# Performance work log

Measured on AMD Instinct MI355X. Metric: run time of the kernel, lower is better.

## Reference

```python
import jax, jax.numpy as jnp
import numpy as np

EPS = 1e-5
C = 1.0
SQRT_C = 1.0
MAX_NORM = 0.95


def _log0(y):
    # log map at origin: atanh(sqrt(c)||y||) * y / (sqrt(c)||y||)
    norm = jnp.clip(jnp.linalg.norm(y, axis=-1, keepdims=True), EPS)
    arg = jnp.clip(SQRT_C * norm, None, 1.0 - EPS)
    return jnp.arctanh(arg) * y / (SQRT_C * norm)


def _exp0(v):
    # exp map at origin: tanh(sqrt(c)||v||) * v / (sqrt(c)||v||)
    norm = jnp.clip(jnp.linalg.norm(v, axis=-1, keepdims=True), EPS)
    return jnp.tanh(SQRT_C * norm) * v / (SQRT_C * norm)


def _proj(x):
    # project onto Poincare ball of radius MAX_NORM/sqrt(c)
    max_r = MAX_NORM / SQRT_C
    norm = jnp.linalg.norm(x, axis=-1, keepdims=True)
    return jnp.where(norm > max_r, x * max_r / jnp.clip(norm, EPS), x)


def _hyp_linear(x, W, b):
    # log -> euclidean linear -> exp -> project
    v = _log0(x)
    v = v @ W.T + b
    return _proj(_exp0(v))


def _hyp_graph_conv(x, src, dst, n_nodes, Wm, bm, Wu, bu):
    # 1. hyperbolic linear message transform
    h = _hyp_linear(x, Wm, bm)
    # 2. tangent-space (hyperbolic) mean aggregation over incoming edges
    t = _log0(h[src])                                   # [E, D]
    summed = jax.ops.segment_sum(t, dst, num_segments=n_nodes)
    cnt = jax.ops.segment_sum(jnp.ones((src.shape[0], 1), t.dtype), dst,
                              num_segments=n_nodes)
    agg = _proj(_exp0(summed / jnp.clip(cnt, 1.0)))
    # 3. hyperbolic linear update
    return _hyp_linear(agg, Wu, bu)


def setup_inputs() -> dict:
    key = jax.random.key(0)
    k1, k2, k3, k4 = jax.random.split(key, 4)
    N, E, D, L = 50000, 800000, 128, 2
    x = jax.random.normal(k1, (N, D), dtype=jnp.float32) * 0.01
    edge_index = jax.random.randint(k2, (2, E), 0, N, dtype=jnp.int32)
    msg_W = jax.random.normal(k3, (L, D, D), dtype=jnp.float32) * 0.05
    msg_b = jnp.zeros((L, D), dtype=jnp.float32)
    upd_W = jax.random.normal(k4, (L, D, D), dtype=jnp.float32) * 0.05
    upd_b = jnp.zeros((L, D), dtype=jnp.float32)
    return {"x": x, "edge_index": edge_index, "msg_W": msg_W, "msg_b": msg_b,
            "upd_W": upd_W, "upd_b": upd_b}


def reference(x, edge_index, msg_W, msg_b, upd_W, upd_b):
    src, dst = edge_index[0], edge_index[1]
    n_nodes = x.shape[0]
    h = x
    for l in range(msg_W.shape[0]):  # small fixed layer count
        h = _hyp_graph_conv(h, src, dst, n_nodes,
                            msg_W[l], msg_b[l], upd_W[l], upd_b[l])
    return h
```

## Files before the change

kernel.cpp:

```cpp
#include <hip/hip_runtime.h>
#include <math.h>

#define EPSF 1e-5f
#define MAXN 0.95f
#define DD 128

typedef unsigned short u16;
typedef __attribute__((ext_vector_type(8))) __bf16 bf16x8;
typedef __attribute__((ext_vector_type(4))) float f32x4;
typedef __attribute__((ext_vector_type(8))) unsigned short u16x8;
typedef __attribute__((ext_vector_type(4))) unsigned u32x4;

#define MFMA16 __builtin_amdgcn_mfma_f32_16x16x32_bf16

__device__ __forceinline__ u16 f2bf(float f) {
    unsigned u = __float_as_uint(f);
    return (u16)((u + 0x7FFFu + ((u >> 16) & 1u)) >> 16);
}
__device__ __forceinline__ float bf2f(u16 b) {
    return __uint_as_float(((unsigned)b) << 16);
}

__device__ __forceinline__ float chain_scale(float nrm, bool log_out) {
    float nc  = fmaxf(nrm, EPSF);
    float f   = tanhf(nc) / nc;
    float wn  = f * nrm;
    float p   = (wn > MAXN) ? (MAXN / fmaxf(wn, EPSF)) : 1.f;
    float s   = f * p;
    if (log_out) {
        float n2  = wn * p;
        float n2c = fmaxf(n2, EPSF);
        float arg = fminf(n2c, 1.f - EPSF);
        s *= atanhf(arg) / n2c;
    }
    return s;
}

__device__ __forceinline__ float agg_scale(const float* __restrict__ ssum,
                                           const int* __restrict__ rowptr,
                                           int rg) {
    int cnt = max(rowptr[rg + 1] - rowptr[rg], 1);
    float inv = 1.f / (float)cnt;
    return chain_scale(sqrtf(ssum[rg]) * inv, true) * inv;
}

__global__ __launch_bounds__(256)
void zero_int4(int4* __restrict__ p, int n4)
{
    int i = blockIdx.x * 256 + threadIdx.x;
    if (i < n4) p[i] = make_int4(0, 0, 0, 0);
}

__global__ __launch_bounds__(256)
void split_w(const float* __restrict__ msgW, const float* __restrict__ updW,
             u16* __restrict__ whi, u16* __restrict__ wlo, int L)
{
    int gid = blockIdx.x * 256 + threadIdx.x;
    int total = L * 2 * DD * DD;
    if (gid >= total) return;
    int mat = gid >> 14;
    int elem = gid & (DD * DD - 1);
    int l = mat >> 1, tpe = mat & 1;
    float f = (tpe ? updW : msgW)[(size_t)l * DD * DD + elem];
    u16 hb = f2bf(f);
    whi[gid] = hb;
    wlo[gid] = f2bf(f - bf2f(hb));
}

template<int LOG_OUT, int FP32_OUT, int F32_IN, int SCALE_IN>
__global__ __launch_bounds__(256)
void mfma_linear(const u16* __restrict__ vhi, const float* __restrict__ xin,
                 const float* __restrict__ ssum, const int* __restrict__ rowptr,
                 const u16* __restrict__ whi, const u16* __restrict__ wlo,
                 const float* __restrict__ bias,
                 u16* __restrict__ ohi, float* __restrict__ ofp, int N)
{
    __shared__ float sred[4][64];
    __shared__ float sScale[64];
    __shared__ float sSin[SCALE_IN ? 64 : 1];
    __shared__ u16 sHi[FP32_OUT ? 1 : 64][136];

    const int tid  = threadIdx.x;
    const int w    = tid >> 6;
    const int lane = tid & 63;
    const int l15  = lane & 15, lk = lane >> 4;
    const int base = blockIdx.x * 64;

    if (SCALE_IN) {
        if (tid < 64) {
            int rg = base + tid;
            sSin[tid] = agg_scale(ssum, rowptr, rg < N ? rg : (N - 1));
        }
        __syncthreads();
    }

    bf16x8 wh[2][4], wl[2][4];
    #pragma unroll
    for (int nt = 0; nt < 2; ++nt) {
        const int j = w * 32 + nt * 16 + l15;
        #pragma unroll
        for (int kt = 0; kt < 4; ++kt) {
            const int off = j * DD + kt * 32 + lk * 8;
            wh[nt][kt] = *(const bf16x8*)(whi + off);
            wl[nt][kt] = *(const bf16x8*)(wlo + off);
        }
    }
    const float bv0 = bias[w * 32 + l15];
    const float bv1 = bias[w * 32 + 16 + l15];

    f32x4 acc[4][2];
    #pragma unroll
    for (int mt = 0; mt < 4; ++mt)
        #pragma unroll
        for (int nt = 0; nt < 2; ++nt)
            acc[mt][nt] = (f32x4){0.f, 0.f, 0.f, 0.f};

    #pragma unroll
    for (int mt = 0; mt < 4; ++mt) {
        int row = base + mt * 16 + l15;
        row = (row < N) ? row : (N - 1);
        bf16x8 ah[4];
        if (F32_IN) {
            const float* xr = xin + (size_t)row * DD + lk * 8;
            float fv[32];
            float ss = 0.f;
            #pragma unroll
            for (int kt = 0; kt < 4; ++kt) {
                float4 a = *(const float4*)(xr + kt * 32);
                float4 b = *(const float4*)(xr + kt * 32 + 4);
                fv[kt*8+0]=a.x; fv[kt*8+1]=a.y; fv[kt*8+2]=a.z; fv[kt*8+3]=a.w;
                fv[kt*8+4]=b.x; fv[kt*8+5]=b.y; fv[kt*8+6]=b.z; fv[kt*8+7]=b.w;
            }
            #pragma unroll
            for (int q = 0; q < 32; ++q) ss += fv[q] * fv[q];
            ss += __shfl_xor(ss, 16);
            ss += __shfl_xor(ss, 32);
            float nc = fmaxf(sqrtf(ss), EPSF);
            float sc = atanhf(fminf(nc, 1.f - EPSF)) / nc;
            #pragma unroll
            for (int kt = 0; kt < 4; ++kt) {
                u16x8 uh;
                #pragma unroll
                for (int q = 0; q < 8; ++q)
                    uh[q] = f2bf(fv[kt*8+q] * sc);
                ah[kt] = *reinterpret_cast<bf16x8*>(&uh);
            }
        } else {
            const size_t ro = (size_t)row * DD + lk * 8;
            #pragma unroll
            for (int kt = 0; kt < 4; ++kt)
                ah[kt] = *(const bf16x8*)(vhi + ro + kt * 32);
        }
        #pragma unroll
        for (int kt = 0; kt < 4; ++kt) {
            #pragma unroll
            for (int nt = 0; nt < 2; ++nt) {
                acc[mt][nt] = MFMA16(ah[kt], wh[nt][kt], acc[mt][nt], 0, 0, 0);
                acc[mt][nt] = MFMA16(ah[kt], wl[nt][kt], acc[mt][nt], 0, 0, 0);
            }
        }
    }

    #pragma unroll
    for (int mt = 0; mt < 4; ++mt) {
        #pragma unroll
        for (int r = 0; r < 4; ++r) {
            const float sv = SCALE_IN ? sSin[mt*16 + lk*4 + r] : 1.f;
            float y0 = acc[mt][0][r] * sv + bv0;
            float y1 = acc[mt][1][r] * sv + bv1;
            float part = y0 * y0 + y1 * y1;
            part += __shfl_xor(part, 1);
            part += __shfl_xor(part, 2);
            part += __shfl_xor(part, 4);
            part += __shfl_xor(part, 8);
            if (l15 == 0) sred[w][mt*16 + lk*4 + r] = part;
        }
    }
    __syncthreads();
    if (tid < 64) {
        float ss = sred[0][tid] + sred[1][tid] + sred[2][tid] + sred[3][tid];
        sScale[tid] = chain_scale(sqrtf(ss), LOG_OUT != 0);
    }
    __syncthreads();

    #pragma unroll
    for (int mt = 0; mt < 4; ++mt) {
        #pragma unroll
        for (int r = 0; r < 4; ++r) {
            const int rloc = mt*16 + lk*4 + r;
            const float s = sScale[rloc];
            const float sv = SCALE_IN ? sSin[rloc] : 1.f;
            #pragma unroll
            for (int nt = 0; nt < 2; ++nt) {
                float z = (acc[mt][nt][r] * sv + (nt ? bv1 : bv0)) * s;
                const int col = w*32 + nt*16 + l15;
                if (FP32_OUT) {
                    const int rg = base + rloc;
                    if (rg < N) ofp[(size_t)rg * DD + col] = z;
                } else {
                    sHi[rloc][col] = f2bf(z);
                }
            }
        }
    }
    if (!FP32_OUT) {
        __syncthreads();
        const int row = tid >> 2, qc = (tid & 3) * 32;
        const int rg = base + row;
        if (rg < N) {
            #pragma unroll
            for (int i = 0; i < 4; ++i)
                *(u16x8*)(ohi + (size_t)rg * DD + qc + i*8) =
                    *(const u16x8*)(&sHi[row][qc + i*8]);
        }
    }
}

__global__ __launch_bounds__(256)
void mfma_linear_fused(const u16* __restrict__ vhi,
                       const float* __restrict__ ssum, const int* __restrict__ rowptr,
                       const u16* __restrict__ wuh, const u16* __restrict__ wul,
                       const float* __restrict__ bu,
                       const u16* __restrict__ wmh, const u16* __restrict__ wml,
                       const float* __restrict__ bm,
                       u16* __restrict__ ohi, int N)
{
    __shared__ float sred[4][64];
    __shared__ float sScale[64];
    __shared__ float sSin[64];
    __shared__ u16 sHi[64][136];

    const int tid  = threadIdx.x;
    const int w    = tid >> 6;
    const int lane = tid & 63;
    const int l15  = lane & 15, lk = lane >> 4;
    const int base = blockIdx.x * 64;

    if (tid < 64) {
        int rg = base + tid;
        sSin[tid] = agg_scale(ssum, rowptr, rg < N ? rg : (N - 1));
    }
    __syncthreads();

    f32x4 acc[4][2];

    {
        bf16x8 wh[2][4], wl[2][4];
        #pragma unroll
        for (int nt = 0; nt < 2; ++nt) {
            const int j = w * 32 + nt * 16 + l15;
            #pragma unroll
            for (int kt = 0; kt < 4; ++kt) {
                const int off = j * DD + kt * 32 + lk * 8;
                wh[nt][kt] = *(const bf16x8*)(wuh + off);
                wl[nt][kt] = *(const bf16x8*)(wul + off);
            }
        }
        const float bv0 = bu[w * 32 + l15];
        const float bv1 = bu[w * 32 + 16 + l15];

        #pragma unroll
        for (int mt = 0; mt < 4; ++mt)
            #pragma unroll
            for (int nt = 0; nt < 2; ++nt)
                acc[mt][nt] = (f32x4){0.f, 0.f, 0.f, 0.f};

        #pragma unroll
        for (int mt = 0; mt < 4; ++mt) {
            int row = base + mt * 16 + l15;
            row = (row < N) ? row : (N - 1);
            const size_t ro = (size_t)row * DD + lk * 8;
            bf16x8 ah[4];
            #pragma unroll
            for (int kt = 0; kt < 4; ++kt)
                ah[kt] = *(const bf16x8*)(vhi + ro + kt * 32);
            #pragma unroll
            for (int kt = 0; kt < 4; ++kt) {
                #pragma unroll
                for (int nt = 0; nt < 2; ++nt) {
                    acc[mt][nt] = MFMA16(ah[kt], wh[nt][kt], acc[mt][nt], 0, 0, 0);
                    acc[mt][nt] = MFMA16(ah[kt], wl[nt][kt], acc[mt][nt], 0, 0, 0);
                }
            }
        }

        #pragma unroll
        for (int mt = 0; mt < 4; ++mt) {
            #pragma unroll
            for (int r = 0; r < 4; ++r) {
                const float sv = sSin[mt*16 + lk*4 + r];
                float y0 = acc[mt][0][r] * sv + bv0;
                float y1 = acc[mt][1][r] * sv + bv1;
                float part = y0 * y0 + y1 * y1;
                part += __shfl_xor(part, 1);
                part += __shfl_xor(part, 2);
                part += __shfl_xor(part, 4);
                part += __shfl_xor(part, 8);
                if (l15 == 0) sred[w][mt*16 + lk*4 + r] = part;
            }
        }
        __syncthreads();
        if (tid < 64) {
            float ss = sred[0][tid] + sred[1][tid] + sred[2][tid] + sred[3][tid];
            sScale[tid] = chain_scale(sqrtf(ss), true);
        }
        __syncthreads();
        #pragma unroll
        for (int mt = 0; mt < 4; ++mt) {
            #pragma unroll
            for (int r = 0; r < 4; ++r) {
                const int rloc = mt*16 + lk*4 + r;
                const float s = sScale[rloc];
                const float sv = sSin[rloc];
                #pragma unroll
                for (int nt = 0; nt < 2; ++nt) {
                    float z = (acc[mt][nt][r] * sv + (nt ? bv1 : bv0)) * s;
                    sHi[rloc][w*32 + nt*16 + l15] = f2bf(z);
                }
            }
        }
    }
    __syncthreads();

    {
        bf16x8 wh[2][4], wl[2][4];
        #pragma unroll
        for (int nt = 0; nt < 2; ++nt) {
            const int j = w * 32 + nt * 16 + l15;
            #pragma unroll
            for (int kt = 0; kt < 4; ++kt) {
                const int off = j * DD + kt * 32 + lk * 8;
                wh[nt][kt] = *(const bf16x8*)(wmh + off);
                wl[nt][kt] = *(const bf16x8*)(wml + off);
            }
        }
        const float bv0 = bm[w * 32 + l15];
        const float bv1 = bm[w * 32 + 16 + l15];

        #pragma unroll
        for (int mt = 0; mt < 4; ++mt)
            #pragma unroll
            for (int nt = 0; nt < 2; ++nt)
                acc[mt][nt] = (f32x4){0.f, 0.f, 0.f, 0.f};

        #pragma unroll
        for (int mt = 0; mt < 4; ++mt) {
            const int r16 = mt * 16 + l15;
            bf16x8 ah[4];
            #pragma unroll
            for (int kt = 0; kt < 4; ++kt)
                ah[kt] = *(const bf16x8*)(&sHi[r16][kt * 32 + lk * 8]);
            #pragma unroll
            for (int kt = 0; kt < 4; ++kt) {
                #pragma unroll
                for (int nt = 0; nt < 2; ++nt) {
                    acc[mt][nt] = MFMA16(ah[kt], wh[nt][kt], acc[mt][nt], 0, 0, 0);
                    acc[mt][nt] = MFMA16(ah[kt], wl[nt][kt], acc[mt][nt], 0, 0, 0);
                }
            }
        }

        #pragma unroll
        for (int mt = 0; mt < 4; ++mt) {
            #pragma unroll
            for (int r = 0; r < 4; ++r) {
                float y0 = acc[mt][0][r] + bv0;
                float y1 = acc[mt][1][r] + bv1;
                float part = y0 * y0 + y1 * y1;
                part += __shfl_xor(part, 1);
                part += __shfl_xor(part, 2);
                part += __shfl_xor(part, 4);
                part += __shfl_xor(part, 8);
                if (l15 == 0) sred[w][mt*16 + lk*4 + r] = part;
            }
        }
        __syncthreads();
        if (tid < 64) {
            float ss = sred[0][tid] + sred[1][tid] + sred[2][tid] + sred[3][tid];
            sScale[tid] = chain_scale(sqrtf(ss), true);
        }
        __syncthreads();
        #pragma unroll
        for (int mt = 0; mt < 4; ++mt) {
            #pragma unroll
            for (int r = 0; r < 4; ++r) {
                const int rloc = mt*16 + lk*4 + r;
                const float s = sScale[rloc];
                #pragma unroll
                for (int nt = 0; nt < 2; ++nt) {
                    float z = (acc[mt][nt][r] + (nt ? bv1 : bv0)) * s;
                    sHi[rloc][w*32 + nt*16 + l15] = f2bf(z);
                }
            }
        }
        __syncthreads();
        const int row = tid >> 2, qc = (tid & 3) * 32;
        const int rg = base + row;
        if (rg < N) {
            #pragma unroll
            for (int i = 0; i < 4; ++i)
                *(u16x8*)(ohi + (size_t)rg * DD + qc + i*8) =
                    *(const u16x8*)(&sHi[row][qc + i*8]);
        }
    }
}

__global__ __launch_bounds__(256)
void degree_rank(const int* __restrict__ dst, int* __restrict__ deg,
                 int* __restrict__ rank, int E)
{
    int e4 = (blockIdx.x * 256 + threadIdx.x) * 4;
    if (e4 + 3 < E) {
        int4 d = *(const int4*)(dst + e4);
        int4 r;
        r.x = atomicAdd(&deg[d.x], 1);
        r.y = atomicAdd(&deg[d.y], 1);
        r.z = atomicAdd(&deg[d.z], 1);
        r.w = atomicAdd(&deg[d.w], 1);
        *(int4*)(rank + e4) = r;
    } else {
        for (int e = e4; e < E; ++e) rank[e] = atomicAdd(&deg[dst[e]], 1);
    }
}

__global__ __launch_bounds__(1024)
void scan_rowptr(const int* __restrict__ deg, int* __restrict__ rowptr, int N)
{
    __shared__ int wsum[16];
    const int t = threadIdx.x, wv = t >> 6, ln = t & 63;
    int carry = 0;
    const int nch = (N + 4095) / 4096;
    for (int c = 0; c < nch; ++c) {
        const int i = c * 4096 + t * 4;
        int4 d = *(const int4*)(deg + i);
        int e1 = d.x, e2 = e1 + d.y, e3 = e2 + d.z, tot = e3 + d.w;
        int sc = tot;
        #pragma unroll
        for (int off = 1; off < 64; off <<= 1) {
            int u = __shfl_up(sc, off);
            if (ln >= off) sc += u;
        }
        if (ln == 63) wsum[wv] = sc;
        __syncthreads();
        if (wv == 0 && ln < 16) {
            int s2 = wsum[ln];
            #pragma unroll
            for (int off = 1; off < 16; off <<= 1) {
                int u = __shfl_up(s2, off);
                if (ln >= off) s2 += u;
            }
            wsum[ln] = s2;
        }
        __syncthreads();
        const int off0 = carry + ((wv > 0) ? wsum[wv - 1] : 0) + (sc - tot);
        if (i + 3 < N) {
            *(int4*)(rowptr + i) = make_int4(off0, off0 + e1, off0 + e2, off0 + e3);
        } else {
            if (i     < N) rowptr[i]     = off0;
            if (i + 1 < N) rowptr[i + 1] = off0 + e1;
            if (i + 2 < N) rowptr[i + 2] = off0 + e2;
        }
        carry += wsum[15];
        __syncthreads();
    }
    if (t == 0) rowptr[N] = carry;
}

__global__ __launch_bounds__(256)
void fill_csr(const int* __restrict__ src, const int* __restrict__ dst,
              const int* __restrict__ rowptr, const int* __restrict__ rank,
              int* __restrict__ csr, int E)
{
    int e4 = (blockIdx.x * 256 + threadIdx.x) * 4;
    if (e4 + 3 < E) {
        int4 d = *(const int4*)(dst + e4);
        int4 r = *(const int4*)(rank + e4);
        int4 s = *(const int4*)(src + e4);
        csr[rowptr[d.x] + r.x] = s.x;
        csr[rowptr[d.y] + r.y] = s.y;
        csr[rowptr[d.z] + r.z] = s.z;
        csr[rowptr[d.w] + r.w] = s.w;
    } else {
        for (int e = e4; e < E; ++e) csr[rowptr[dst[e]] + rank[e]] = src[e];
    }
}

__global__ __launch_bounds__(256)
void csr_gather_sum(const u16* __restrict__ ghi, const int* __restrict__ rowptr,
                    const int* __restrict__ csr, u16* __restrict__ ohi,
                    float* __restrict__ ssum, int N)
{
    int node = blockIdx.x * 4 + (threadIdx.x >> 6);
    if (node >= N) return;
    const int lane = threadIdx.x & 63;
    const int eg = lane >> 4, l15 = lane & 15;
    const int beg = rowptr[node], end = rowptr[node + 1];

    float acc[8] = {0.f,0.f,0.f,0.f,0.f,0.f,0.f,0.f};
    for (int b = beg; b < end; b += 64) {
        const int cnt = min(end - b, 64);
        const int myidx = (lane < cnt) ? csr[b + lane] : 0;
        u32x4 vc;
        {
            const bool act = eg < cnt;
            const int s = __shfl(myidx, act ? eg : 0);
            if (act) vc = *(const u32x4*)(ghi + (size_t)s * DD + l15 * 8);
        }
        for (int j = 0; j < cnt; j += 4) {
            const int en = j + 4 + eg;
            const bool actn = en < cnt;
            const int sn = __shfl(myidx, actn ? en : 0);
            u32x4 vn;
            if (actn) vn = *(const u32x4*)(ghi + (size_t)sn * DD + l15 * 8);
            if (j + eg < cnt) {
                #pragma unroll
                for (int p = 0; p < 4; ++p) {
                    acc[2*p+0] += __uint_as_float(vc[p] << 16);
                    acc[2*p+1] += __uint_as_float(vc[p] & 0xffff0000u);
                }
            }
            vc = vn;
        }
    }
    #pragma unroll
    for (int q = 0; q < 8; ++q) {
        acc[q] += __shfl_xor(acc[q], 16);
        acc[q] += __shfl_xor(acc[q], 32);
    }
    float ss = 0.f;
    #pragma unroll
    for (int q = 0; q < 8; ++q) ss += acc[q] * acc[q];
    ss += __shfl_xor(ss, 1); ss += __shfl_xor(ss, 2);
    ss += __shfl_xor(ss, 4); ss += __shfl_xor(ss, 8);
    if (eg == 0) {
        u32x4 hw;
        #pragma unroll
        for (int p = 0; p < 4; ++p) {
            u16 h0 = f2bf(acc[2*p+0]), h1 = f2bf(acc[2*p+1]);
            hw[p] = (unsigned)h0 | ((unsigned)h1 << 16);
        }
        *(u32x4*)(ohi + (size_t)node * DD + l15 * 8) = hw;
        if (l15 == 0) ssum[node] = ss;
    }
}

extern "C" void kernel_launch(void* const* d_in, const int* in_sizes, int n_in,
                              void* d_out, int out_size, void* d_ws, size_t ws_size,
                              hipStream_t stream)
{
    const float* x     = (const float*)d_in[0];
    const int*   ei    = (const int*)d_in[1];
    const float* msg_W = (const float*)d_in[2];
    const float* msg_b = (const float*)d_in[3];
    const float* upd_W = (const float*)d_in[4];
    const float* upd_b = (const float*)d_in[5];

    const int N = in_sizes[0] / DD;
    const int E = in_sizes[1] / 2;
    const int L = in_sizes[2] / (DD * DD);

    const int* src = ei;
    const int* dst = ei + E;

    u16* Ahi  = (u16*)d_ws;
    u16* WhiA = Ahi + (size_t)N * DD;
    u16* WloA = WhiA + (size_t)2 * L * DD * DD;
    int* deg  = (int*)(WloA + (size_t)2 * L * DD * DD);
    const int degCap = ((N + 4095) / 4096) * 4096;
    int* rowptr = deg + degCap;
    int* csr    = rowptr + (N + 1);
    float* ssum = (float*)(csr + E);

    u16* Bhi  = (u16*)d_out;
    int* rank = (int*)(Bhi + (size_t)N * DD);

    const int nodeBlocks  = (N + 63) / 64;
    const int aggBlocks   = (N + 3) / 4;
    const int edge4Blocks = ((E + 3) / 4 + 255) / 256;

    zero_int4<<<(degCap / 4 + 255) / 256, 256, 0, stream>>>((int4*)deg, degCap / 4);
    degree_rank<<<edge4Blocks, 256, 0, stream>>>(dst, deg, rank, E);
    scan_rowptr<<<1, 1024, 0, stream>>>(deg, rowptr, N);
    fill_csr<<<edge4Blocks, 256, 0, stream>>>(src, dst, rowptr, rank, csr, E);
    split_w<<<(2 * L * DD * DD + 255) / 256, 256, 0, stream>>>(
        msg_W, upd_W, WhiA, WloA, L);

    mfma_linear<1, 0, 1, 0><<<nodeBlocks, 256, 0, stream>>>(
        nullptr, x, nullptr, nullptr,
        WhiA, WloA, msg_b, Bhi, nullptr, N);

    for (int l = 0; l < L; ++l) {
        const u16* wuh = WhiA + (size_t)(l * 2 + 1) * DD * DD;
        const u16* wul = WloA + (size_t)(l * 2 + 1) * DD * DD;

        csr_gather_sum<<<aggBlocks, 256, 0, stream>>>(
            Bhi, rowptr, csr, Ahi, ssum, N);

        if (l < L - 1) {
            const u16* wmh = WhiA + (size_t)((l + 1) * 2 + 0) * DD * DD;
            const u16* wml = WloA + (size_t)((l + 1) * 2 + 0) * DD * DD;
            mfma_linear_fused<<<nodeBlocks, 256, 0, stream>>>(
                Ahi, ssum, rowptr,
                wuh, wul, upd_b + (size_t)l * DD,
                wmh, wml, msg_b + (size_t)(l + 1) * DD,
                Bhi, N);
        } else {
            mfma_linear<0, 1, 0, 1><<<nodeBlocks, 256, 0, stream>>>(
                Ahi, nullptr, ssum, rowptr,
                wuh, wul, upd_b + (size_t)l * DD,
                nullptr, (float*)d_out, N);
        }
    }
}
```

Baseline: 237.5 us.

## Build CSR with 16-bit packed edges and per-block shared-memory histograms

When N fits in 16 bits, edge indices are first packed to u16. Degree counting and CSR fill then run in 64 blocks, and each block scans all edges but owns one contiguous node range. Counts go through shared-memory atomics instead of global atomics, and no per-edge rank array is written. Each block rereads the full packed edge list, so total reads rise about 64-fold, and only 64 blocks are used. Fill order within a row becomes nondeterministic.

```diff
diff --git a/kernel.cpp b/kernel.cpp
--- a/kernel.cpp
+++ b/kernel.cpp
@@ -4,6 +4,7 @@
 #define EPSF 1e-5f
 #define MAXN 0.95f
 #define DD 128
+#define HBLK 64
 
 typedef unsigned short u16;
 typedef __attribute__((ext_vector_type(8))) __bf16 bf16x8;
@@ -405,6 +406,89 @@
     }
 }
 
+__global__ __launch_bounds__(512)
+void pack_u16(const int* __restrict__ ei, u16* __restrict__ s16,
+              u16* __restrict__ d16, int E)
+{
+    int e4 = (blockIdx.x * 512 + threadIdx.x) * 4;
+    if (e4 + 3 < E) {
+        int4 s = *(const int4*)(ei + e4);
+        int4 d = *(const int4*)(ei + E + e4);
+        ushort4 sp; sp.x = (u16)s.x; sp.y = (u16)s.y; sp.z = (u16)s.z; sp.w = (u16)s.w;
+        ushort4 dp; dp.x = (u16)d.x; dp.y = (u16)d.y; dp.z = (u16)d.z; dp.w = (u16)d.w;
+        *(ushort4*)(s16 + e4) = sp;
+        *(ushort4*)(d16 + e4) = dp;
+    } else {
+        for (int e = e4; e < E; ++e) {
+            s16[e] = (u16)ei[e];
+            d16[e] = (u16)ei[E + e];
+        }
+    }
+}
+
+__global__ __launch_bounds__(512)
+void deg_hist(const u16* __restrict__ d16, int* __restrict__ deg, int E, int N)
+{
+    __shared__ int hist[1032];
+    const int R  = (N + HBLK - 1) / HBLK;
+    const int lo = blockIdx.x * R;
+    const int hi = min(lo + R, N);
+    for (int j = threadIdx.x; j < R; j += 512) hist[j] = 0;
+    __syncthreads();
+    const int E8 = E >> 3;
+    for (int i = threadIdx.x; i < E8; i += 512) {
+        u16x8 v = *(const u16x8*)(d16 + i * 8);
+        #pragma unroll
+        for (int q = 0; q < 8; ++q) {
+            int d = v[q];
+            if (d >= lo && d < hi) atomicAdd(&hist[d - lo], 1);
+        }
+    }
+    for (int e = E8 * 8 + threadIdx.x; e < E; e += 512) {
+        int d = d16[e];
+        if (d >= lo && d < hi) atomicAdd(&hist[d - lo], 1);
+    }
+    __syncthreads();
+    for (int j = threadIdx.x; j < hi - lo; j += 512) deg[lo + j] = hist[j];
+}
+
+__global__ __launch_bounds__(512)
+void fill_hist(const u16* __restrict__ d16, const u16* __restrict__ s16,
+               const int* __restrict__ rowptr, int* __restrict__ csr,
+               int E, int N)
+{
+    __shared__ int rp[1032];
+    __shared__ int cnt[1032];
+    const int R  = (N + HBLK - 1) / HBLK;
+    const int lo = blockIdx.x * R;
+    const int hi = min(lo + R, N);
+    for (int j = threadIdx.x; j < hi - lo; j += 512) {
+        rp[j]  = rowptr[lo + j];
+        cnt[j] = 0;
+    }
+    __syncthreads();
+    const int E8 = E >> 3;
+    for (int i = threadIdx.x; i < E8; i += 512) {
+        u16x8 d = *(const u16x8*)(d16 + i * 8);
+        u16x8 s = *(const u16x8*)(s16 + i * 8);
+        #pragma unroll
+        for (int q = 0; q < 8; ++q) {
+            int dd = d[q];
+            if (dd >= lo && dd < hi) {
+                int pos = rp[dd - lo] + atomicAdd(&cnt[dd - lo], 1);
+                csr[pos] = (int)s[q];
+            }
+        }
+    }
+    for (int e = E8 * 8 + threadIdx.x; e < E; e += 512) {
+        int dd = d16[e];
+        if (dd >= lo && dd < hi) {
+            int pos = rp[dd - lo] + atomicAdd(&cnt[dd - lo], 1);
+            csr[pos] = (int)s16[e];
+        }
+    }
+}
+
 __global__ __launch_bounds__(256)
 void degree_rank(const int* __restrict__ dst, int* __restrict__ deg,
                  int* __restrict__ rank, int E)
@@ -423,49 +507,6 @@
     }
 }
 
-__global__ __launch_bounds__(1024)
-void scan_rowptr(const int* __restrict__ deg, int* __restrict__ rowptr, int N)
-{
-    __shared__ int wsum[16];
-    const int t = threadIdx.x, wv = t >> 6, ln = t & 63;
-    int carry = 0;
-    const int nch = (N + 4095) / 4096;
-    for (int c = 0; c < nch; ++c) {
-        const int i = c * 4096 + t * 4;
-        int4 d = *(const int4*)(deg + i);
-        int e1 = d.x, e2 = e1 + d.y, e3 = e2 + d.z, tot = e3 + d.w;
-        int sc = tot;
-        #pragma unroll
-        for (int off = 1; off < 64; off <<= 1) {
-            int u = __shfl_up(sc, off);
-            if (ln >= off) sc += u;
-        }
-        if (ln == 63) wsum[wv] = sc;
-        __syncthreads();
-        if (wv == 0 && ln < 16) {
-            int s2 = wsum[ln];
-            #pragma unroll
-            for (int off = 1; off < 16; off <<= 1) {
-                int u = __shfl_up(s2, off);
-                if (ln >= off) s2 += u;
-            }
-            wsum[ln] = s2;
-        }
-        __syncthreads();
-        const int off0 = carry + ((wv > 0) ? wsum[wv - 1] : 0) + (sc - tot);
-        if (i + 3 < N) {
-            *(int4*)(rowptr + i) = make_int4(off0, off0 + e1, off0 + e2, off0 + e3);
-        } else {
-            if (i     < N) rowptr[i]     = off0;
-            if (i + 1 < N) rowptr[i + 1] = off0 + e1;
-            if (i + 2 < N) rowptr[i + 2] = off0 + e2;
-        }
-        carry += wsum[15];
-        __syncthreads();
-    }
-    if (t == 0) rowptr[N] = carry;
-}
-
 __global__ __launch_bounds__(256)
 void fill_csr(const int* __restrict__ src, const int* __restrict__ dst,
               const int* __restrict__ rowptr, const int* __restrict__ rank,
@@ -483,6 +524,49 @@
     } else {
         for (int e = e4; e < E; ++e) csr[rowptr[dst[e]] + rank[e]] = src[e];
     }
+}
+
+__global__ __launch_bounds__(1024)
+void scan_rowptr(const int* __restrict__ deg, int* __restrict__ rowptr, int N)
+{
+    __shared__ int wsum[16];
+    const int t = threadIdx.x, wv = t >> 6, ln = t & 63;
+    int carry = 0;
+    const int nch = (N + 4095) / 4096;
+    for (int c = 0; c < nch; ++c) {
+        const int i = c * 4096 + t * 4;
+        int4 d = *(const int4*)(deg + i);
+        int e1 = d.x, e2 = e1 + d.y, e3 = e2 + d.z, tot = e3 + d.w;
+        int sc = tot;
+        #pragma unroll
+        for (int off = 1; off < 64; off <<= 1) {
+            int u = __shfl_up(sc, off);
+            if (ln >= off) sc += u;
+        }
+        if (ln == 63) wsum[wv] = sc;
+        __syncthreads();
+        if (wv == 0 && ln < 16) {
+            int s2 = wsum[ln];
+            #pragma unroll
+            for (int off = 1; off < 16; off <<= 1) {
+                int u = __shfl_up(s2, off);
+                if (ln >= off) s2 += u;
+            }
+            wsum[ln] = s2;
+        }
+        __syncthreads();
+        const int off0 = carry + ((wv > 0) ? wsum[wv - 1] : 0) + (sc - tot);
+        if (i + 3 < N) {
+            *(int4*)(rowptr + i) = make_int4(off0, off0 + e1, off0 + e2, off0 + e3);
+        } else {
+            if (i     < N) rowptr[i]     = off0;
+            if (i + 1 < N) rowptr[i + 1] = off0 + e1;
+            if (i + 2 < N) rowptr[i + 2] = off0 + e2;
+        }
+        carry += wsum[15];
+        __syncthreads();
+    }
+    if (t == 0) rowptr[N] = carry;
 }
 
 __global__ __launch_bounds__(256)
@@ -570,6 +654,8 @@
     int* rowptr = deg + degCap;
     int* csr    = rowptr + (N + 1);
     float* ssum = (float*)(csr + E);
+    u16* d16    = (u16*)(ssum + N);
+    u16* s16    = d16 + E;
 
     u16* Bhi  = (u16*)d_out;
     int* rank = (int*)(Bhi + (size_t)N * DD);
@@ -577,11 +663,22 @@
     const int nodeBlocks  = (N + 63) / 64;
     const int aggBlocks   = (N + 3) / 4;
     const int edge4Blocks = ((E + 3) / 4 + 255) / 256;
-
-    zero_int4<<<(degCap / 4 + 255) / 256, 256, 0, stream>>>((int4*)deg, degCap / 4);
-    degree_rank<<<edge4Blocks, 256, 0, stream>>>(dst, deg, rank, E);
-    scan_rowptr<<<1, 1024, 0, stream>>>(deg, rowptr, N);
-    fill_csr<<<edge4Blocks, 256, 0, stream>>>(src, dst, rowptr, rank, csr, E);
+    const bool u16ok = (N <= 65535) && ((N + HBLK - 1) / HBLK <= 1032);
+
+    if (u16ok) {
+        const int padStart4 = (N & ~3) / 4;
+        zero_int4<<<(degCap / 4 - padStart4 + 255) / 256, 256, 0, stream>>>(
+            (int4*)deg + padStart4, degCap / 4 - padStart4);
+        pack_u16<<<((E + 3) / 4 + 511) / 512, 512, 0, stream>>>(ei, s16, d16, E);
+        deg_hist<<<HBLK, 512, 0, stream>>>(d16, deg, E, N);
+        scan_rowptr<<<1, 1024, 0, stream>>>(deg, rowptr, N);
+        fill_hist<<<HBLK, 512, 0, stream>>>(d16, s16, rowptr, csr, E, N);
+    } else {
+        zero_int4<<<(degCap / 4 + 255) / 256, 256, 0, stream>>>((int4*)deg, degCap / 4);
+        degree_rank<<<edge4Blocks, 256, 0, stream>>>(dst, deg, rank, E);
+        scan_rowptr<<<1, 1024, 0, stream>>>(deg, rowptr, N);
+        fill_csr<<<edge4Blocks, 256, 0, stream>>>(src, dst, rowptr, rank, csr, E);
+    }
     split_w<<<(2 * L * DD * DD + 255) / 256, 256, 0, stream>>>(
         msg_W, upd_W, WhiA, WloA, L);
 
```

Result: slower. 483.7 us (+103.6%).
